# Performance work log

Measured on AMD Instinct MI355X. Metric: run time of the kernel, lower is better.

Reference implementation:

```python
import jax, jax.numpy as jnp
import numpy as np

T, B, N, DIN, DOUT = 300, 64, 512, 10, 2
ALPHA = 0.2


def setup_inputs() -> dict:
    key = jax.random.key(0)
    ks = jax.random.split(key, 16)
    sN = 1.0 / float(np.sqrt(N))
    sI = 1.0 / float(np.sqrt(DIN))
    sO = 1.0 / float(np.sqrt(DOUT))
    g = lambda k, shape, s: jax.random.normal(k, shape, dtype=jnp.float32) * s
    return {
        "stim": jax.random.normal(ks[0], (T, B, DIN), dtype=jnp.float32),
        # recurrent weights (one per region)
        "W_rec_m1": g(ks[1], (N, N), sN),
        "W_rec_pmd": g(ks[2], (N, N), sN),
        "W_rec_s1": g(ks[3], (N, N), sN),
        # region -> region connections (Linear with bias)
        "W_pmd_m1": g(ks[4], (N, N), sN), "b_pmd_m1": jnp.zeros((N,), jnp.float32),
        "W_m1_pmd": g(ks[5], (N, N), sN), "b_m1_pmd": jnp.zeros((N,), jnp.float32),
        "W_s1_pmd": g(ks[6], (N, N), sN), "b_s1_pmd": jnp.zeros((N,), jnp.float32),
        # input -> S1
        "W_in_s1": g(ks[7], (DIN, N), sI), "b_in_s1": jnp.zeros((N,), jnp.float32),
        # M1 -> output readout
        "W_out_m1": g(ks[8], (N, DOUT), sN), "b_out_m1": jnp.zeros((DOUT,), jnp.float32),
        # output feedback -> PMd
        "W_fb_pmd": g(ks[9], (DOUT, N), sO), "b_fb_pmd": jnp.zeros((N,), jnp.float32),
    }


def reference(stim, W_rec_m1, W_rec_pmd, W_rec_s1,
              W_pmd_m1, b_pmd_m1, W_m1_pmd, b_m1_pmd, W_s1_pmd, b_s1_pmd,
              W_in_s1, b_in_s1, W_out_m1, b_out_m1, W_fb_pmd, b_fb_pmd):
    Bsz = stim.shape[1]
    x0 = jnp.zeros((Bsz, N), jnp.float32)      # zero hidden-state init
    out0 = jnp.zeros((Bsz, DOUT), jnp.float32)  # output reset value at t=0

    def step(carry, u_t):
        x_m1, x_pmd, x_s1, out_prev = carry
        # rates at t-1
        r_m1, r_pmd, r_s1 = jnp.tanh(x_m1), jnp.tanh(x_pmd), jnp.tanh(x_s1)
        # accumulate messages into each region's inputs_at_current_time
        in_m1 = r_pmd @ W_pmd_m1 + b_pmd_m1
        in_pmd = ((r_m1 @ W_m1_pmd + b_m1_pmd)
                  + (r_s1 @ W_s1_pmd + b_s1_pmd)
                  + (out_prev @ W_fb_pmd + b_fb_pmd))
        in_s1 = u_t @ W_in_s1 + b_in_s1
        # leaky recurrent update (f_step): x <- (1-a)x + a(W_rec r + input)
        x_m1n = (1.0 - ALPHA) * x_m1 + ALPHA * (r_m1 @ W_rec_m1 + in_m1)
        x_pmdn = (1.0 - ALPHA) * x_pmd + ALPHA * (r_pmd @ W_rec_pmd + in_pmd)
        x_s1n = (1.0 - ALPHA) * x_s1 + ALPHA * (r_s1 @ W_rec_s1 + in_s1)
        r_m1n = jnp.tanh(x_m1n)
        r_pmdn = jnp.tanh(x_pmdn)
        r_s1n = jnp.tanh(x_s1n)
        # output uses rates at current time t
        out_t = r_m1n @ W_out_m1 + b_out_m1
        return (x_m1n, x_pmdn, x_s1n, out_t), (r_m1n, r_pmdn, r_s1n, out_t)

    # torch loop runs t = 1 .. T-1, driven by inputs[t]
    _, (r_m1s, r_pmds, r_s1s, outs) = jax.lax.scan(step, (x0, x0, x0, out0), stim[1:])

    zN = jnp.zeros((1, Bsz, N), jnp.float32)   # rates[0] = tanh(0) = 0
    r_m1_full = jnp.concatenate([zN, r_m1s], axis=0)
    r_pmd_full = jnp.concatenate([zN, r_pmds], axis=0)
    r_s1_full = jnp.concatenate([zN, r_s1s], axis=0)
    outs_full = jnp.concatenate([out0[None], outs], axis=0)  # [T, B, DOUT]
    return outs_full, r_m1_full, r_pmd_full, r_s1_full
```

## Files before the change

### kernel.cpp

```cpp
#include <hip/hip_runtime.h>

#define TSTEPS 300
#define OFF_RM1  38400
#define RSTRIDE  9830400

#define DOMS 8
#define DROWS 8
#define CPD 24
#define NBLK 200
#define THREADS 512
#define PAD 520
#define PSTR (DROWS*PAD)

typedef float f4 __attribute__((ext_vector_type(4)));
typedef unsigned long long u64;

#define WS_INTS 128

__device__ __forceinline__ void publish16(float* p, f4 v) {
  union { f4 f; u64 q[2]; } u; u.f = v;
  __hip_atomic_store((u64*)p,       u.q[0], __ATOMIC_RELAXED, __HIP_MEMORY_SCOPE_AGENT);
  __hip_atomic_store(((u64*)p) + 1, u.q[1], __ATOMIC_RELAXED, __HIP_MEMORY_SCOPE_AGENT);
}

__device__ __forceinline__ void out_dot(const float* rrow, const float* W_out,
                                        float& o0, float& o1) {
  const int lane = threadIdx.x & 63;
  f4 ra = *(const f4*)(rrow + lane * 8);
  f4 rb = *(const f4*)(rrow + lane * 8 + 4);
  f4 w0 = *(const f4*)(W_out + lane * 16);
  f4 w1 = *(const f4*)(W_out + lane * 16 + 4);
  f4 w2 = *(const f4*)(W_out + lane * 16 + 8);
  f4 w3 = *(const f4*)(W_out + lane * 16 + 12);
  o0 = ra.x*w0.x + ra.y*w0.z + ra.z*w1.x + ra.w*w1.z
     + rb.x*w2.x + rb.y*w2.z + rb.z*w3.x + rb.w*w3.z;
  o1 = ra.x*w0.y + ra.y*w0.w + ra.z*w1.y + ra.w*w1.w
     + rb.x*w2.y + rb.y*w2.w + rb.z*w3.y + rb.w*w3.w;
  #pragma unroll
  for (int m = 1; m < 64; m <<= 1) {
    o0 += __shfl_xor(o0, m, 64);
    o1 += __shfl_xor(o1, m, 64);
  }
}

__global__ __launch_bounds__(256) void rnn_init(float* ws, float* dout) {
  int gid = blockIdx.x * blockDim.x + threadIdx.x;
  int stride = gridDim.x * blockDim.x;
  int* wi = (int*)ws;
  for (int i = gid; i < WS_INTS; i += stride) wi[i] = 0;
  for (int i = gid; i < 128; i += stride) dout[i] = 0.f;
  for (int i = gid; i < 3 * 32768; i += stride) {
    int rr = i >> 15, j = i & 32767;
    dout[OFF_RM1 + (size_t)rr * RSTRIDE + j] = 0.f;
  }
}

__global__ __launch_bounds__(THREADS, 1) void rnn_persist(
    const float* __restrict__ stim,
    const float* __restrict__ W_rec_m1, const float* __restrict__ W_rec_pmd,
    const float* __restrict__ W_rec_s1,
    const float* __restrict__ W_pmd_m1, const float* __restrict__ b_pmd_m1,
    const float* __restrict__ W_m1_pmd, const float* __restrict__ b_m1_pmd,
    const float* __restrict__ W_s1_pmd, const float* __restrict__ b_s1_pmd,
    const float* __restrict__ W_in_s1,  const float* __restrict__ b_in_s1,
    const float* __restrict__ W_out_m1, const float* __restrict__ b_out_m1,
    const float* __restrict__ W_fb_pmd, const float* __restrict__ b_fb_pmd,
    float* __restrict__ ws, float* __restrict__ dout)
{
  __shared__ float panel[3 * PSTR];
  __shared__ f4    scr[3 * 128];
  __shared__ float o_lds[16];

  const int blk = blockIdx.x;
  const int tid = threadIdx.x;
  const int dom = blk & 7;
  const int sub = blk >> 3;
  int* ctr = (int*)ws + dom * 16;

  const float* rates0 = dout + OFF_RM1;
  const int rowbase = dom * DROWS;

  if (sub == 24) {
    const int wave = tid >> 6;
    const int lane = tid & 63;
    for (int t = 1; t < TSTEPS; ++t) {
      if (tid == 0) {
        while (__hip_atomic_load(ctr, __ATOMIC_RELAXED, __HIP_MEMORY_SCOPE_AGENT) < CPD * t)
          __builtin_amdgcn_s_sleep(2);
      }
      __syncthreads();
      const int row = rowbase + wave;
      float o0, o1;
      out_dot(rates0 + (size_t)t * 32768 + row * 512, W_out_m1, o0, o1);
      if (lane == 0) {
        dout[(size_t)t * 128 + row * 2]     = o0 + b_out_m1[0];
        dout[(size_t)t * 128 + row * 2 + 1] = o1 + b_out_m1[1];
      }
      __syncthreads();
    }
    return;
  }

  const int region = sub >> 3;
  const int c    = sub & 7;
  const int task = tid >> 7;
  const int s    = tid & 127;
  const int bb   = s >> 4;
  const int nq   = s & 15;
  const int n    = c * 64 + nq * 4;
  const int row  = rowbase + bb;

  const float *WA, *WB = nullptr, *WC = nullptr;
  int nseg, KQ;
  if (region == 0)      { WA = W_rec_m1;  WB = W_pmd_m1;                  nseg = 2; KQ = 256; }
  else if (region == 1) { WA = W_rec_pmd; WB = W_m1_pmd; WC = W_s1_pmd;   nseg = 3; KQ = 384; }
  else                  { WA = W_rec_s1;                                  nseg = 1; KQ = 128; }

  f4 bias, fb0 = {0,0,0,0}, fb1 = {0,0,0,0};
  if (region == 0) bias = *(const f4*)(b_pmd_m1 + n);
  else if (region == 1) {
    bias  = *(const f4*)(b_m1_pmd + n);
    bias += *(const f4*)(b_s1_pmd + n);
    bias += *(const f4*)(b_fb_pmd + n);
    fb0 = *(const f4*)(W_fb_pmd + n);
    fb1 = *(const f4*)(W_fb_pmd + 512 + n);
  } else bias = *(const f4*)(b_in_s1 + n);

  const int nseg2 = nseg * 2;
  f4 xv = {0.f, 0.f, 0.f, 0.f};

  for (int t = 1; t < TSTEPS; ++t) {
    const float* rb_ = dout + OFF_RM1 + (size_t)(t - 1) * 32768 + rowbase * 512;
    const float *src0, *src1 = nullptr, *src2 = nullptr;
    if (region == 0)      { src0 = rb_;                    src1 = rb_ + RSTRIDE; }
    else if (region == 1) { src0 = rb_ + RSTRIDE;          src1 = rb_;
                            src2 = rb_ + 2 * (size_t)RSTRIDE; }
    else                  { src0 = rb_ + 2 * (size_t)RSTRIDE; }

    {
      f4 tmp[6];
      #pragma unroll
      for (int i = 0; i < 6; ++i) {
        if (i < nseg2) {
          int j = tid + i * 512;
          int p = j >> 10, idx = j & 1023;
          const float* sp = (p == 0) ? src0 : (p == 1) ? src1 : src2;
          tmp[i] = *(const f4*)(sp + (idx >> 7) * 512 + (idx & 127) * 4);
        }
      }
      #pragma unroll
      for (int i = 0; i < 6; ++i) {
        if (i < nseg2) {
          int j = tid + i * 512;
          int p = j >> 10, idx = j & 1023;
          *(f4*)(panel + p * PSTR + (idx >> 7) * PAD + (idx & 127) * 4) = tmp[i];
        }
      }
    }
    __syncthreads();

    f4 acc = {0.f, 0.f, 0.f, 0.f};
    {
      int K = task * KQ, Khi = K + KQ;
      while (K < Khi) {
        int seg  = K >> 9;
        int kend = (seg + 1) << 9; if (kend > Khi) kend = Khi;
        const float* wg  = ((seg == 0) ? WA : (seg == 1) ? WB : WC)
                         + (size_t)(K & 511) * 512 + n;
        const float* pan = panel + seg * PSTR + bb * PAD + (K & 511);
        #pragma unroll 2
        for (int k = K; k < kend; k += 4) {
          f4 r  = *(const f4*)pan; pan += 4;
          f4 g0 = *(const f4*)(wg);
          f4 g1 = *(const f4*)(wg + 512);
          f4 g2 = *(const f4*)(wg + 1024);
          f4 g3 = *(const f4*)(wg + 1536);
          wg += 2048;
          acc += r.x * g0; acc += r.y * g1; acc += r.z * g2; acc += r.w * g3;
        }
        K = kend;
      }
    }

    if (region == 1) {
      const int wave = tid >> 6;
      float o0, o1;
      out_dot(panel + PSTR + wave * PAD, W_out_m1, o0, o1);
      if ((tid & 63) == 0) {
        o_lds[wave * 2]     = o0 + b_out_m1[0];
        o_lds[wave * 2 + 1] = o1 + b_out_m1[1];
      }
    }

    if (task > 0) scr[(task - 1) * 128 + s] = acc;
    __syncthreads();

    if (task == 0) {
      f4 pre = acc + scr[s] + scr[128 + s] + scr[256 + s] + bias;
      if (region == 1) {
        if (t >= 2) {
          float o0 = o_lds[bb * 2], o1 = o_lds[bb * 2 + 1];
          pre += o0 * fb0;
          pre += o1 * fb1;
        }
      } else if (region == 2) {
        const float* u = stim + (size_t)t * 640 + row * 10;
        #pragma unroll
        for (int j = 0; j < 10; ++j)
          pre += u[j] * *(const f4*)(W_in_s1 + j * 512 + n);
      }
      xv = 0.8f * xv + 0.2f * pre;
      f4 rv = {tanhf(xv.x), tanhf(xv.y), tanhf(xv.z), tanhf(xv.w)};
      publish16(dout + OFF_RM1 + (size_t)region * RSTRIDE + (size_t)t * 32768
                + row * 512 + n, rv);
    }

    __syncthreads();
    if (tid == 0) {
      __hip_atomic_fetch_add(ctr, 1, __ATOMIC_RELAXED, __HIP_MEMORY_SCOPE_AGENT);
      if (t < TSTEPS - 1) {
        while (__hip_atomic_load(ctr, __ATOMIC_RELAXED, __HIP_MEMORY_SCOPE_AGENT) < CPD * t)
          __builtin_amdgcn_s_sleep(1);
      }
    }
    __syncthreads();
  }
}

extern "C" void kernel_launch(void* const* d_in, const int* in_sizes, int n_in,
                              void* d_out, int out_size, void* d_ws, size_t ws_size,
                              hipStream_t stream) {
  const float* stim      = (const float*)d_in[0];
  const float* W_rec_m1  = (const float*)d_in[1];
  const float* W_rec_pmd = (const float*)d_in[2];
  const float* W_rec_s1  = (const float*)d_in[3];
  const float* W_pmd_m1  = (const float*)d_in[4];
  const float* b_pmd_m1  = (const float*)d_in[5];
  const float* W_m1_pmd  = (const float*)d_in[6];
  const float* b_m1_pmd  = (const float*)d_in[7];
  const float* W_s1_pmd  = (const float*)d_in[8];
  const float* b_s1_pmd  = (const float*)d_in[9];
  const float* W_in_s1   = (const float*)d_in[10];
  const float* b_in_s1   = (const float*)d_in[11];
  const float* W_out_m1  = (const float*)d_in[12];
  const float* b_out_m1  = (const float*)d_in[13];
  const float* W_fb_pmd  = (const float*)d_in[14];
  const float* b_fb_pmd  = (const float*)d_in[15];

  float* ws   = (float*)d_ws;
  float* dout = (float*)d_out;

  hipLaunchKernelGGL(rnn_init, dim3(256), dim3(256), 0, stream, ws, dout);

  void* args[] = {
    (void*)&stim,
    (void*)&W_rec_m1, (void*)&W_rec_pmd, (void*)&W_rec_s1,
    (void*)&W_pmd_m1, (void*)&b_pmd_m1,
    (void*)&W_m1_pmd, (void*)&b_m1_pmd,
    (void*)&W_s1_pmd, (void*)&b_s1_pmd,
    (void*)&W_in_s1,  (void*)&b_in_s1,
    (void*)&W_out_m1, (void*)&b_out_m1,
    (void*)&W_fb_pmd, (void*)&b_fb_pmd,
    (void*)&ws, (void*)&dout
  };
  hipLaunchCooperativeKernel((const void*)rnn_persist, dim3(NBLK), dim3(THREADS),
                             args, 0, stream);
}
```

Baseline: 9.651 ms.

## Repartition persistent RNN by source region with block-to-block partial-sum exchange

Work is now split by source region instead of destination region. Each block loads only its own region's previous rates (16 batch rows), computes the cross-region message product and publishes it to workspace with a per-block flag, then computes its own recurrent product while the peer blocks finish. Consumer blocks spin on those flags and add the exchanged partial sums. This balances the K work per block (every block does 512+512 instead of 512 to 1536) and cuts redundant panel loads. In exchange it adds extra flag waits and global round-trips for the partial sums on every step.

```diff
diff --git a/kernel.cpp b/kernel.cpp
--- a/kernel.cpp
+++ b/kernel.cpp
@@ -4,23 +4,32 @@
 #define OFF_RM1  38400
 #define RSTRIDE  9830400
 
-#define DOMS 8
-#define DROWS 8
+#define DOMS 4
+#define DROWS 16
 #define CPD 24
-#define NBLK 200
+#define NBLK 128
 #define THREADS 512
-#define PAD 520
-#define PSTR (DROWS*PAD)
+#define PAD 516
+
+#define WS_INT_F 98304
+#define WS_INTS  1600
+#define WS_TOTAL 99904
 
 typedef float f4 __attribute__((ext_vector_type(4)));
 typedef unsigned long long u64;
-
-#define WS_INTS 128
 
 __device__ __forceinline__ void publish16(float* p, f4 v) {
   union { f4 f; u64 q[2]; } u; u.f = v;
   __hip_atomic_store((u64*)p,       u.q[0], __ATOMIC_RELAXED, __HIP_MEMORY_SCOPE_AGENT);
   __hip_atomic_store(((u64*)p) + 1, u.q[1], __ATOMIC_RELAXED, __HIP_MEMORY_SCOPE_AGENT);
+}
+__device__ __forceinline__ f4 fetch4(const float* p) {
+  f4 v;
+  v.x = __hip_atomic_load(p + 0, __ATOMIC_RELAXED, __HIP_MEMORY_SCOPE_AGENT);
+  v.y = __hip_atomic_load(p + 1, __ATOMIC_RELAXED, __HIP_MEMORY_SCOPE_AGENT);
+  v.z = __hip_atomic_load(p + 2, __ATOMIC_RELAXED, __HIP_MEMORY_SCOPE_AGENT);
+  v.w = __hip_atomic_load(p + 3, __ATOMIC_RELAXED, __HIP_MEMORY_SCOPE_AGENT);
+  return v;
 }
 
 __device__ __forceinline__ void out_dot(const float* rrow, const float* W_out,
@@ -46,7 +55,7 @@
 __global__ __launch_bounds__(256) void rnn_init(float* ws, float* dout) {
   int gid = blockIdx.x * blockDim.x + threadIdx.x;
   int stride = gridDim.x * blockDim.x;
-  int* wi = (int*)ws;
+  int* wi = (int*)(ws + WS_INT_F);
   for (int i = gid; i < WS_INTS; i += stride) wi[i] = 0;
   for (int i = gid; i < 128; i += stride) dout[i] = 0.f;
   for (int i = gid; i < 3 * 32768; i += stride) {
@@ -67,143 +76,196 @@
     const float* __restrict__ W_fb_pmd, const float* __restrict__ b_fb_pmd,
     float* __restrict__ ws, float* __restrict__ dout)
 {
-  __shared__ float panel[3 * PSTR];
-  __shared__ f4    scr[3 * 128];
-  __shared__ float o_lds[16];
+  __shared__ float panel[DROWS * PAD];
+  __shared__ f4    scr[256];
+  __shared__ float o_lds[32];
 
   const int blk = blockIdx.x;
   const int tid = threadIdx.x;
-  const int dom = blk & 7;
-  const int sub = blk >> 3;
-  int* ctr = (int*)ws + dom * 16;
-
-  const float* rates0 = dout + OFF_RM1;
-  const int rowbase = dom * DROWS;
-
-  if (sub == 24) {
-    const int wave = tid >> 6;
-    const int lane = tid & 63;
+  const int x = blk & 7;
+  const int jj = blk >> 3;
+
+  int* ibase = (int*)(ws + WS_INT_F);
+
+  if (x == 6) {
+    if (jj >= DOMS) return;
+    const int dom = jj;
+    const int rowbase = dom * DROWS;
+    int* ctr = ibase + 1536 + dom * 16;
+    const float* rates0 = dout + OFF_RM1;
+    const int wave = tid >> 6, lane = tid & 63;
     for (int t = 1; t < TSTEPS; ++t) {
       if (tid == 0) {
         while (__hip_atomic_load(ctr, __ATOMIC_RELAXED, __HIP_MEMORY_SCOPE_AGENT) < CPD * t)
           __builtin_amdgcn_s_sleep(2);
       }
       __syncthreads();
-      const int row = rowbase + wave;
-      float o0, o1;
-      out_dot(rates0 + (size_t)t * 32768 + row * 512, W_out_m1, o0, o1);
-      if (lane == 0) {
-        dout[(size_t)t * 128 + row * 2]     = o0 + b_out_m1[0];
-        dout[(size_t)t * 128 + row * 2 + 1] = o1 + b_out_m1[1];
+      #pragma unroll
+      for (int h = 0; h < 2; ++h) {
+        int rr = rowbase + wave + h * 8;
+        float o0, o1;
+        out_dot(rates0 + (size_t)t * 32768 + rr * 512, W_out_m1, o0, o1);
+        if (lane == 0) {
+          dout[(size_t)t * 128 + rr * 2]     = o0 + b_out_m1[0];
+          dout[(size_t)t * 128 + rr * 2 + 1] = o1 + b_out_m1[1];
+        }
       }
       __syncthreads();
     }
     return;
   }
-
-  const int region = sub >> 3;
-  const int c    = sub & 7;
-  const int task = tid >> 7;
-  const int s    = tid & 127;
+  if (x == 7 || jj >= 16) return;
+
+  const int src = x >> 1;
+  const int dom = (x & 1) + 2 * (jj >> 3);
+  const int c   = jj & 7;
+  const int rowbase = dom * DROWS;
+
+  const int task = tid >> 8;
+  const int s    = tid & 255;
   const int bb   = s >> 4;
   const int nq   = s & 15;
   const int n    = c * 64 + nq * 4;
   const int row  = rowbase + bb;
 
-  const float *WA, *WB = nullptr, *WC = nullptr;
-  int nseg, KQ;
-  if (region == 0)      { WA = W_rec_m1;  WB = W_pmd_m1;                  nseg = 2; KQ = 256; }
-  else if (region == 1) { WA = W_rec_pmd; WB = W_m1_pmd; WC = W_s1_pmd;   nseg = 3; KQ = 384; }
-  else                  { WA = W_rec_s1;                                  nseg = 1; KQ = 128; }
-
-  f4 bias, fb0 = {0,0,0,0}, fb1 = {0,0,0,0};
-  if (region == 0) bias = *(const f4*)(b_pmd_m1 + n);
-  else if (region == 1) {
+  const float *Wown, *Wexp;
+  if (src == 0)      { Wown = W_rec_m1;  Wexp = W_m1_pmd; }
+  else if (src == 1) { Wown = W_rec_pmd; Wexp = W_pmd_m1; }
+  else               { Wown = W_rec_s1;  Wexp = W_s1_pmd; }
+
+  f4 bias, fbv0 = {0,0,0,0}, fbv1 = {0,0,0,0};
+  if (src == 0) {
+    bias = *(const f4*)(b_pmd_m1 + n);
+    fbv0 = *(const f4*)(W_fb_pmd + n);
+    fbv1 = *(const f4*)(W_fb_pmd + 512 + n);
+  } else if (src == 1) {
     bias  = *(const f4*)(b_m1_pmd + n);
     bias += *(const f4*)(b_s1_pmd + n);
     bias += *(const f4*)(b_fb_pmd + n);
-    fb0 = *(const f4*)(W_fb_pmd + n);
-    fb1 = *(const f4*)(W_fb_pmd + 512 + n);
   } else bias = *(const f4*)(b_in_s1 + n);
 
-  const int nseg2 = nseg * 2;
+  float* Pexp = ws + ((size_t)(dom * 3 + src) * 8 + c) * 1024;
+  float* Prd0 = ws + ((size_t)(dom * 3 + ((src == 0) ? 1 : 0)) * 8 + c) * 1024;
+  float* Prd2 = ws + ((size_t)(dom * 3 + 2) * 8 + c) * 1024;
+  int* myflag = ibase + ((dom * 3 + src) * 8 + c) * 16;
+  int* rdf0   = ibase + ((dom * 3 + ((src == 0) ? 1 : 0)) * 8 + c) * 16;
+  int* rdf2   = ibase + ((dom * 3 + 2) * 8 + c) * 16;
+  int* ctr    = ibase + 1536 + dom * 16;
+  const int off = bb * 64 + nq * 4;
+
   f4 xv = {0.f, 0.f, 0.f, 0.f};
 
   for (int t = 1; t < TSTEPS; ++t) {
-    const float* rb_ = dout + OFF_RM1 + (size_t)(t - 1) * 32768 + rowbase * 512;
-    const float *src0, *src1 = nullptr, *src2 = nullptr;
-    if (region == 0)      { src0 = rb_;                    src1 = rb_ + RSTRIDE; }
-    else if (region == 1) { src0 = rb_ + RSTRIDE;          src1 = rb_;
-                            src2 = rb_ + 2 * (size_t)RSTRIDE; }
-    else                  { src0 = rb_ + 2 * (size_t)RSTRIDE; }
-
     {
-      f4 tmp[6];
-      #pragma unroll
-      for (int i = 0; i < 6; ++i) {
-        if (i < nseg2) {
-          int j = tid + i * 512;
-          int p = j >> 10, idx = j & 1023;
-          const float* sp = (p == 0) ? src0 : (p == 1) ? src1 : src2;
-          tmp[i] = *(const f4*)(sp + (idx >> 7) * 512 + (idx & 127) * 4);
-        }
-      }
-      #pragma unroll
-      for (int i = 0; i < 6; ++i) {
-        if (i < nseg2) {
-          int j = tid + i * 512;
-          int p = j >> 10, idx = j & 1023;
-          *(f4*)(panel + p * PSTR + (idx >> 7) * PAD + (idx & 127) * 4) = tmp[i];
-        }
-      }
-    }
-    __syncthreads();
-
-    f4 acc = {0.f, 0.f, 0.f, 0.f};
+      const float* srcp = dout + OFF_RM1 + (size_t)src * RSTRIDE
+                        + (size_t)(t - 1) * 32768 + rowbase * 512;
+      f4 tmp[4];
+      #pragma unroll
+      for (int i = 0; i < 4; ++i) {
+        int j2 = tid + i * 512;
+        tmp[i] = *(const f4*)(srcp + (j2 >> 7) * 512 + (j2 & 127) * 4);
+      }
+      #pragma unroll
+      for (int i = 0; i < 4; ++i) {
+        int j2 = tid + i * 512;
+        *(f4*)(panel + (j2 >> 7) * PAD + (j2 & 127) * 4) = tmp[i];
+      }
+    }
+    __syncthreads();
+
+    if (src == 0 && t >= 2) {
+      int rr = tid >> 5, kc = tid & 31;
+      const float* pr = panel + rr * PAD;
+      float o0 = 0.f, o1 = 0.f;
+      #pragma unroll
+      for (int i = 0; i < 4; ++i) {
+        int k = kc * 4 + i * 128;
+        f4 r  = *(const f4*)(pr + k);
+        f4 wa = *(const f4*)(W_out_m1 + k * 2);
+        f4 wb = *(const f4*)(W_out_m1 + k * 2 + 4);
+        o0 += r.x*wa.x + r.y*wa.z + r.z*wb.x + r.w*wb.z;
+        o1 += r.x*wa.y + r.y*wa.w + r.z*wb.y + r.w*wb.w;
+      }
+      #pragma unroll
+      for (int m = 1; m < 32; m <<= 1) {
+        o0 += __shfl_xor(o0, m, 64);
+        o1 += __shfl_xor(o1, m, 64);
+      }
+      if ((tid & 31) == 0) {
+        o_lds[rr * 2]     = o0 + b_out_m1[0];
+        o_lds[rr * 2 + 1] = o1 + b_out_m1[1];
+      }
+    }
+
+    f4 acc;
     {
-      int K = task * KQ, Khi = K + KQ;
-      while (K < Khi) {
-        int seg  = K >> 9;
-        int kend = (seg + 1) << 9; if (kend > Khi) kend = Khi;
-        const float* wg  = ((seg == 0) ? WA : (seg == 1) ? WB : WC)
-                         + (size_t)(K & 511) * 512 + n;
-        const float* pan = panel + seg * PSTR + bb * PAD + (K & 511);
-        #pragma unroll 2
-        for (int k = K; k < kend; k += 4) {
-          f4 r  = *(const f4*)pan; pan += 4;
-          f4 g0 = *(const f4*)(wg);
-          f4 g1 = *(const f4*)(wg + 512);
-          f4 g2 = *(const f4*)(wg + 1024);
-          f4 g3 = *(const f4*)(wg + 1536);
-          wg += 2048;
-          acc += r.x * g0; acc += r.y * g1; acc += r.z * g2; acc += r.w * g3;
-        }
-        K = kend;
-      }
-    }
-
-    if (region == 1) {
-      const int wave = tid >> 6;
-      float o0, o1;
-      out_dot(panel + PSTR + wave * PAD, W_out_m1, o0, o1);
-      if ((tid & 63) == 0) {
-        o_lds[wave * 2]     = o0 + b_out_m1[0];
-        o_lds[wave * 2 + 1] = o1 + b_out_m1[1];
-      }
-    }
-
-    if (task > 0) scr[(task - 1) * 128 + s] = acc;
-    __syncthreads();
-
+      const float* wg  = Wexp + (size_t)(task * 256) * 512 + n;
+      const float* pan = panel + bb * PAD + task * 256;
+      f4 a = {0.f, 0.f, 0.f, 0.f};
+      #pragma unroll 2
+      for (int kk = 0; kk < 256; kk += 4) {
+        f4 r  = *(const f4*)(pan + kk);
+        f4 g0 = *(const f4*)(wg);
+        f4 g1 = *(const f4*)(wg + 512);
+        f4 g2 = *(const f4*)(wg + 1024);
+        f4 g3 = *(const f4*)(wg + 1536);
+        wg += 2048;
+        a += r.x * g0; a += r.y * g1; a += r.z * g2; a += r.w * g3;
+      }
+      acc = a;
+    }
+    if (task == 1) scr[s] = acc;
+    __syncthreads();
     if (task == 0) {
-      f4 pre = acc + scr[s] + scr[128 + s] + scr[256 + s] + bias;
-      if (region == 1) {
-        if (t >= 2) {
-          float o0 = o_lds[bb * 2], o1 = o_lds[bb * 2 + 1];
-          pre += o0 * fb0;
-          pre += o1 * fb1;
-        }
-      } else if (region == 2) {
+      f4 pe = acc + scr[s];
+      if (src == 0 && t >= 2) {
+        pe += o_lds[bb * 2]     * fbv0;
+        pe += o_lds[bb * 2 + 1] * fbv1;
+      }
+      publish16(Pexp + off, pe);
+    }
+    __syncthreads();
+    if (tid == 0)
+      __hip_atomic_fetch_add(myflag, 1, __ATOMIC_RELAXED, __HIP_MEMORY_SCOPE_AGENT);
+
+    {
+      const float* wg  = Wown + (size_t)(task * 256) * 512 + n;
+      const float* pan = panel + bb * PAD + task * 256;
+      f4 a = {0.f, 0.f, 0.f, 0.f};
+      #pragma unroll 2
+      for (int kk = 0; kk < 256; kk += 4) {
+        f4 r  = *(const f4*)(pan + kk);
+        f4 g0 = *(const f4*)(wg);
+        f4 g1 = *(const f4*)(wg + 512);
+        f4 g2 = *(const f4*)(wg + 1024);
+        f4 g3 = *(const f4*)(wg + 1536);
+        wg += 2048;
+        a += r.x * g0; a += r.y * g1; a += r.z * g2; a += r.w * g3;
+      }
+      acc = a;
+    }
+    if (task == 1) scr[s] = acc;
+    if (tid == 0) {
+      if (src == 0) {
+        while (__hip_atomic_load(rdf0, __ATOMIC_RELAXED, __HIP_MEMORY_SCOPE_AGENT) < t)
+          __builtin_amdgcn_s_sleep(1);
+      } else if (src == 1) {
+        while (__hip_atomic_load(rdf0, __ATOMIC_RELAXED, __HIP_MEMORY_SCOPE_AGENT) < t)
+          __builtin_amdgcn_s_sleep(1);
+        while (__hip_atomic_load(rdf2, __ATOMIC_RELAXED, __HIP_MEMORY_SCOPE_AGENT) < t)
+          __builtin_amdgcn_s_sleep(1);
+      }
+    }
+    __syncthreads();
+
+    if (task == 0) {
+      f4 pre = acc + scr[s] + bias;
+      if (src == 0) {
+        pre += fetch4(Prd0 + off);
+      } else if (src == 1) {
+        pre += fetch4(Prd0 + off);
+        pre += fetch4(Prd2 + off);
+      } else {
         const float* u = stim + (size_t)t * 640 + row * 10;
         #pragma unroll
         for (int j = 0; j < 10; ++j)
@@ -211,7 +273,7 @@
       }
       xv = 0.8f * xv + 0.2f * pre;
       f4 rv = {tanhf(xv.x), tanhf(xv.y), tanhf(xv.z), tanhf(xv.w)};
-      publish16(dout + OFF_RM1 + (size_t)region * RSTRIDE + (size_t)t * 32768
+      publish16(dout + OFF_RM1 + (size_t)src * RSTRIDE + (size_t)t * 32768
                 + row * 512 + n, rv);
     }
 
```

Result: no change. 9.602 ms (-0.5%).
